# Kernel optimization log

Hardware: AMD Instinct MI355X
Metric: run time of the kernel (lower is better)

## Reference

```python
import jax, jax.numpy as jnp
import numpy as np

NUM_CLASSES = 21
EPS = 1e-06


def setup_inputs() -> dict:
    key = jax.random.key(0)
    k1, k2 = jax.random.split(key)
    predictions = jax.random.normal(k1, (16, NUM_CLASSES, 512, 512), dtype=jnp.float32)
    targets = jax.random.randint(k2, (16, 512, 512), 0, NUM_CLASSES, dtype=jnp.int32)
    return {"predictions": predictions, "targets": targets}


def reference(predictions, targets):
    C = NUM_CLASSES
    # argmax over channel dim -> [B, H, W] predicted class ids
    pred = jnp.argmax(predictions, axis=1).ravel()
    tgt = targets.ravel().astype(pred.dtype)
    ones = jnp.ones_like(pred, dtype=jnp.float32)
    # single-pass histogram counts (the fused form of the per-class loop)
    pred_cnt = jnp.zeros((C,), jnp.float32).at[pred].add(ones)
    tgt_cnt = jnp.zeros((C,), jnp.float32).at[tgt].add(ones)
    # intersection: count positions where pred == tgt == c; route mismatches to bin C
    inter_idx = jnp.where(pred == tgt, pred, C)
    inter = jnp.zeros((C + 1,), jnp.float32).at[inter_idx].add(ones)[:C]
    union = pred_cnt + tgt_cnt - inter  # == count((pred_mask + tgt_mask) > 0)
    iou = jnp.where(union > 0, inter / (union + EPS), 0.0)
    return jnp.mean(iou)
```

## Files before the change

### kernel.cpp

```cpp
#include <hip/hip_runtime.h>

#define NUM_CLASSES 21
#define HW4   65536
#define NGRP  1048576

__global__ __launch_bounds__(256) void iou_hist_kernel(
    const float4* __restrict__ pred, const int4* __restrict__ tgt,
    unsigned int* __restrict__ hist) {
  __shared__ unsigned int sh[3 * NUM_CLASSES];
  const int tid = threadIdx.x;
  if (tid < 3 * NUM_CLASSES) sh[tid] = 0;
  __syncthreads();

  const int lane = tid & 63;
  unsigned int cp = 0, ct = 0, ci = 0;

  const int gstart  = blockIdx.x * blockDim.x + tid;
  const int gstride = gridDim.x * blockDim.x;

  for (int g = gstart; g < NGRP; g += gstride) {
    const int b    = g >> 16;
    const int hw4  = g & (HW4 - 1);
    const int base = b * NUM_CLASSES;

    float4 best = pred[(base << 16) + hw4];
    int i0 = 0, i1 = 0, i2 = 0, i3 = 0;
#pragma unroll
    for (int c = 1; c < NUM_CLASSES; ++c) {
      float4 v = pred[((base + c) << 16) + hw4];
      if (v.x > best.x) { best.x = v.x; i0 = c; }
      if (v.y > best.y) { best.y = v.y; i1 = c; }
      if (v.z > best.z) { best.z = v.z; i2 = c; }
      if (v.w > best.w) { best.w = v.w; i3 = c; }
    }

    const int4 t = tgt[g];

#pragma unroll
    for (int c = 0; c < NUM_CLASSES; ++c) {
      unsigned int np_ = (unsigned)__popcll(__ballot(i0 == c))
                       + (unsigned)__popcll(__ballot(i1 == c))
                       + (unsigned)__popcll(__ballot(i2 == c))
                       + (unsigned)__popcll(__ballot(i3 == c));
      unsigned int nt_ = (unsigned)__popcll(__ballot(t.x == c))
                       + (unsigned)__popcll(__ballot(t.y == c))
                       + (unsigned)__popcll(__ballot(t.z == c))
                       + (unsigned)__popcll(__ballot(t.w == c));
      unsigned int ni_ = (unsigned)__popcll(__ballot(i0 == c && t.x == c))
                       + (unsigned)__popcll(__ballot(i1 == c && t.y == c))
                       + (unsigned)__popcll(__ballot(i2 == c && t.z == c))
                       + (unsigned)__popcll(__ballot(i3 == c && t.w == c));
      if (lane == c) { cp += np_; ct += nt_; ci += ni_; }
    }
  }

  if (lane < NUM_CLASSES) {
    atomicAdd(&sh[lane], cp);
    atomicAdd(&sh[NUM_CLASSES + lane], ct);
    atomicAdd(&sh[2 * NUM_CLASSES + lane], ci);
  }
  __syncthreads();
  if (tid < 3 * NUM_CLASSES) atomicAdd(&hist[tid], sh[tid]);
}

__global__ __launch_bounds__(64) void iou_finalize_kernel(
    const unsigned int* __restrict__ hist, float* __restrict__ out) {
  const int lane = threadIdx.x;
  float iou = 0.0f;
  if (lane < NUM_CLASSES) {
    const float p = (float)hist[lane];
    const float t = (float)hist[NUM_CLASSES + lane];
    const float i = (float)hist[2 * NUM_CLASSES + lane];
    const float u = p + t - i;
    iou = (u > 0.0f) ? (i / (u + 1e-6f)) : 0.0f;
  }
#pragma unroll
  for (int off = 32; off > 0; off >>= 1) iou += __shfl_down(iou, off);
  if (lane == 0) out[0] = iou / (float)NUM_CLASSES;
}

extern "C" void kernel_launch(void* const* d_in, const int* in_sizes, int n_in,
                              void* d_out, int out_size, void* d_ws, size_t ws_size,
                              hipStream_t stream) {
  const float4* pred = (const float4*)d_in[0];
  const int4*   tgt  = (const int4*)d_in[1];
  float*        out  = (float*)d_out;
  unsigned int* hist = (unsigned int*)d_ws;

  hipMemsetAsync(d_ws, 0, 3 * NUM_CLASSES * sizeof(unsigned int), stream);

  iou_hist_kernel<<<2048, 256, 0, stream>>>(pred, tgt, hist);
  iou_finalize_kernel<<<1, 64, 0, stream>>>(hist, out);
}
```

Baseline: 100.0 us.

## Use one group per thread with batched nontemporal loads and cheaper intersection ballots

```diff
diff --git a/kernel.cpp b/kernel.cpp
--- a/kernel.cpp
+++ b/kernel.cpp
@@ -4,8 +4,11 @@
 #define HW4   65536
 #define NGRP  1048576
 
+typedef float f4 __attribute__((ext_vector_type(4)));
+typedef int   i4 __attribute__((ext_vector_type(4)));
+
 __global__ __launch_bounds__(256) void iou_hist_kernel(
-    const float4* __restrict__ pred, const int4* __restrict__ tgt,
+    const f4* __restrict__ pred, const i4* __restrict__ tgt,
     unsigned int* __restrict__ hist) {
   __shared__ unsigned int sh[3 * NUM_CLASSES];
   const int tid = threadIdx.x;
@@ -13,45 +16,54 @@
   __syncthreads();
 
   const int lane = tid & 63;
+  const int g    = blockIdx.x * 256 + tid;
+  const int b    = g >> 16;
+  const int hw4  = g & (HW4 - 1);
+  const int base = (b * NUM_CLASSES) << 16;
+
+  f4 best = __builtin_nontemporal_load(&pred[base + hw4]);
+  int i0 = 0, i1 = 0, i2 = 0, i3 = 0;
+
+#pragma unroll
+  for (int cc = 1; cc < NUM_CLASSES; cc += 5) {
+    f4 v[5];
+#pragma unroll
+    for (int j = 0; j < 5; ++j)
+      v[j] = __builtin_nontemporal_load(&pred[base + ((cc + j) << 16) + hw4]);
+#pragma unroll
+    for (int j = 0; j < 5; ++j) {
+      const int c = cc + j;
+      if (v[j][0] > best[0]) { best[0] = v[j][0]; i0 = c; }
+      if (v[j][1] > best[1]) { best[1] = v[j][1]; i1 = c; }
+      if (v[j][2] > best[2]) { best[2] = v[j][2]; i2 = c; }
+      if (v[j][3] > best[3]) { best[3] = v[j][3]; i3 = c; }
+    }
+  }
+
+  const i4 t = __builtin_nontemporal_load(&tgt[g]);
+
+  const unsigned long long m0 = __ballot(i0 == t[0]);
+  const unsigned long long m1 = __ballot(i1 == t[1]);
+  const unsigned long long m2 = __ballot(i2 == t[2]);
+  const unsigned long long m3 = __ballot(i3 == t[3]);
+
   unsigned int cp = 0, ct = 0, ci = 0;
 
-  const int gstart  = blockIdx.x * blockDim.x + tid;
-  const int gstride = gridDim.x * blockDim.x;
-
-  for (int g = gstart; g < NGRP; g += gstride) {
-    const int b    = g >> 16;
-    const int hw4  = g & (HW4 - 1);
-    const int base = b * NUM_CLASSES;
-
-    float4 best = pred[(base << 16) + hw4];
-    int i0 = 0, i1 = 0, i2 = 0, i3 = 0;
 #pragma unroll
-    for (int c = 1; c < NUM_CLASSES; ++c) {
-      float4 v = pred[((base + c) << 16) + hw4];
-      if (v.x > best.x) { best.x = v.x; i0 = c; }
-      if (v.y > best.y) { best.y = v.y; i1 = c; }
-      if (v.z > best.z) { best.z = v.z; i2 = c; }
-      if (v.w > best.w) { best.w = v.w; i3 = c; }
-    }
-
-    const int4 t = tgt[g];
-
-#pragma unroll
-    for (int c = 0; c < NUM_CLASSES; ++c) {
-      unsigned int np_ = (unsigned)__popcll(__ballot(i0 == c))
-                       + (unsigned)__popcll(__ballot(i1 == c))
-                       + (unsigned)__popcll(__ballot(i2 == c))
-                       + (unsigned)__popcll(__ballot(i3 == c));
-      unsigned int nt_ = (unsigned)__popcll(__ballot(t.x == c))
-                       + (unsigned)__popcll(__ballot(t.y == c))
-                       + (unsigned)__popcll(__ballot(t.z == c))
-                       + (unsigned)__popcll(__ballot(t.w == c));
-      unsigned int ni_ = (unsigned)__popcll(__ballot(i0 == c && t.x == c))
-                       + (unsigned)__popcll(__ballot(i1 == c && t.y == c))
-                       + (unsigned)__popcll(__ballot(i2 == c && t.z == c))
-                       + (unsigned)__popcll(__ballot(i3 == c && t.w == c));
-      if (lane == c) { cp += np_; ct += nt_; ci += ni_; }
-    }
+  for (int c = 0; c < NUM_CLASSES; ++c) {
+    const unsigned long long p0 = __ballot(i0 == c);
+    const unsigned long long p1 = __ballot(i1 == c);
+    const unsigned long long p2 = __ballot(i2 == c);
+    const unsigned long long p3 = __ballot(i3 == c);
+    const unsigned int np_ = (unsigned)__popcll(p0) + (unsigned)__popcll(p1)
+                           + (unsigned)__popcll(p2) + (unsigned)__popcll(p3);
+    const unsigned int ni_ = (unsigned)__popcll(p0 & m0) + (unsigned)__popcll(p1 & m1)
+                           + (unsigned)__popcll(p2 & m2) + (unsigned)__popcll(p3 & m3);
+    const unsigned int nt_ = (unsigned)__popcll(__ballot(t[0] == c))
+                           + (unsigned)__popcll(__ballot(t[1] == c))
+                           + (unsigned)__popcll(__ballot(t[2] == c))
+                           + (unsigned)__popcll(__ballot(t[3] == c));
+    if (lane == c) { cp = np_; ct = nt_; ci = ni_; }
   }
 
   if (lane < NUM_CLASSES) {
@@ -82,13 +94,13 @@
 extern "C" void kernel_launch(void* const* d_in, const int* in_sizes, int n_in,
                               void* d_out, int out_size, void* d_ws, size_t ws_size,
                               hipStream_t stream) {
-  const float4* pred = (const float4*)d_in[0];
-  const int4*   tgt  = (const int4*)d_in[1];
-  float*        out  = (float*)d_out;
+  const f4* pred = (const f4*)d_in[0];
+  const i4* tgt  = (const i4*)d_in[1];
+  float*    out  = (float*)d_out;
   unsigned int* hist = (unsigned int*)d_ws;
 
   hipMemsetAsync(d_ws, 0, 3 * NUM_CLASSES * sizeof(unsigned int), stream);
 
-  iou_hist_kernel<<<2048, 256, 0, stream>>>(pred, tgt, hist);
+  iou_hist_kernel<<<NGRP / 256, 256, 0, stream>>>(pred, tgt, hist);
   iou_finalize_kernel<<<1, 64, 0, stream>>>(hist, out);
 }
```

Measured after the change: 102.8 us. 2.8% more time.
